# Kernel optimization log

Measured on AMD Instinct MI355X. Metric: run time of the kernel, lower is better.

The kernel has to match this reference:

```python
import jax, jax.numpy as jnp
import numpy as np

D_MODEL = 1024
NUM_HEADS = 16
D_K = D_MODEL // NUM_HEADS
SCALE = float(np.sqrt(D_K))


def setup_inputs() -> dict:
    key = jax.random.key(0)
    ks = jax.random.split(key, 11)
    B, S, D = 4, 2048, D_MODEL
    w_std = 1.0 / np.sqrt(D)
    inp = {
        "query": jax.random.normal(ks[0], (B, S, D), jnp.float32),
        "key": jax.random.normal(ks[1], (B, S, D), jnp.float32),
        "value": jax.random.normal(ks[2], (B, S, D), jnp.float32),
        "wq": jax.random.normal(ks[3], (D, D), jnp.float32) * w_std,
        "bq": jax.random.normal(ks[4], (D,), jnp.float32) * w_std,
        "wk": jax.random.normal(ks[5], (D, D), jnp.float32) * w_std,
        "bk": jax.random.normal(ks[6], (D,), jnp.float32) * w_std,
        "wv": jax.random.normal(ks[7], (D, D), jnp.float32) * w_std,
        "bv": jax.random.normal(ks[8], (D,), jnp.float32) * w_std,
        "wo": jax.random.normal(ks[9], (D, D), jnp.float32) * w_std,
        "bo": jax.random.normal(ks[10], (D,), jnp.float32) * w_std,
    }
    return inp


def reference(query, key, value, wq, bq, wk, bk, wv, bv, wo, bo):
    B, Sq, D = query.shape
    H, dk = NUM_HEADS, D_K
    # linear projections (weights stored as [in, out])
    q = query @ wq + bq
    k = key @ wk + bk
    v = value @ wv + bv
    # [B, H, S, d_k]
    q = q.reshape(B, Sq, H, dk).transpose(0, 2, 1, 3)
    k = k.reshape(B, -1, H, dk).transpose(0, 2, 1, 3)
    v = v.reshape(B, -1, H, dk).transpose(0, 2, 1, 3)
    # full attention scores [B, H, Sq, Sk]
    att = jnp.einsum("bhqd,bhkd->bhqk", q, k) / SCALE
    att = jax.nn.softmax(att, axis=-1)
    out = jnp.einsum("bhqk,bhkd->bhqd", att, v)
    out = out.transpose(0, 2, 1, 3).reshape(B, Sq, D)
    return out @ wo + bo
```

## Files before the change

### kernel.cpp

```cpp
#include <hip/hip_runtime.h>


typedef _Float16 fp16;
typedef fp16  fp16x8 __attribute__((ext_vector_type(8)));
typedef fp16  fp16x4 __attribute__((ext_vector_type(4)));
typedef float f32x4  __attribute__((ext_vector_type(4)));

#define NROWS 8192
#define DM    1024
#define SEQ   2048
#define DK    64
#define LOG2E 1.44269504088896340736f
#define QSCALE (0.125f * LOG2E)

__device__ __forceinline__ f32x4 mfma16x16(fp16x8 a, fp16x8 b, f32x4 c) {
    return __builtin_amdgcn_mfma_f32_16x16x32_f16(a, b, c, 0, 0, 0);
}

__device__ __forceinline__ void gload16(const void* g, void* l) {
    __builtin_amdgcn_global_load_lds(
        (const __attribute__((address_space(1))) void*)g,
        (__attribute__((address_space(3))) void*)l, 16, 0, 0);
}

__global__ __launch_bounds__(256) void cast_fp16_kernel(
    const float* __restrict__ x0, const float* __restrict__ x1,
    const float* __restrict__ x2,
    fp16* __restrict__ y0, fp16* __restrict__ y1, fp16* __restrict__ y2,
    int n4) {
    const int z = blockIdx.y;
    const float* x = (z == 0) ? x0 : (z == 1) ? x1 : x2;
    fp16*       y = (z == 0) ? y0 : (z == 1) ? y1 : y2;
    int i = blockIdx.x * 256 + threadIdx.x;
    if (i >= n4) return;
    const float4 v = ((const float4*)x)[i];
    fp16x4 o;
    o[0] = (fp16)v.x; o[1] = (fp16)v.y; o[2] = (fp16)v.z; o[3] = (fp16)v.w;
    ((fp16x4*)y)[i] = o;
}

__global__ __launch_bounds__(256) void transpose_w_kernel(
    const float* __restrict__ w0, const float* __restrict__ w1,
    const float* __restrict__ w2, const float* __restrict__ w3,
    fp16* __restrict__ t0, fp16* __restrict__ t1,
    fp16* __restrict__ t2, fp16* __restrict__ t3) {
    const int z = blockIdx.z;
    const float* W = (z == 0) ? w0 : (z == 1) ? w1 : (z == 2) ? w2 : w3;
    fp16*       T = (z == 0) ? t0 : (z == 1) ? t1 : (z == 2) ? t2 : t3;
    __shared__ float tile[32][33];
    const int tx = threadIdx.x, ty = threadIdx.y;
    const int bx = blockIdx.x * 32, by = blockIdx.y * 32;
#pragma unroll
    for (int j = 0; j < 4; ++j)
        tile[ty + 8 * j][tx] = W[(size_t)(by + ty + 8 * j) * DM + bx + tx];
    __syncthreads();
#pragma unroll
    for (int j = 0; j < 4; ++j)
        T[(size_t)(bx + ty + 8 * j) * DM + by + tx] = (fp16)tile[tx][ty + 8 * j];
}

__global__ __launch_bounds__(256) void gemm_qkv_kernel(
    const fp16* __restrict__ Xq, const fp16* __restrict__ Xk,
    const fp16* __restrict__ Xv,
    const fp16* __restrict__ Wq, const fp16* __restrict__ Wk,
    const fp16* __restrict__ Wv,
    const float* __restrict__ bq, const float* __restrict__ bk,
    const float* __restrict__ bv,
    fp16* __restrict__ Qb, fp16* __restrict__ Kb, fp16* __restrict__ Vtg) {
    const int i = blockIdx.x;
    const int xcd = i & 7, r = i >> 3;
    const int z = r >> 6, rr = r & 63;
    const int m0 = (xcd * 8 + (rr >> 3)) * 128;
    const int n0 = (rr & 7) * 128;

    const fp16* __restrict__ A = (z == 0) ? Xq : (z == 1) ? Xk : Xv;
    const fp16* __restrict__ B = (z == 0) ? Wq : (z == 1) ? Wk : Wv;
    const float* __restrict__ bias = (z == 0) ? bq : (z == 1) ? bk : bv;
    fp16* __restrict__ outp = (z == 0) ? Qb : (z == 1) ? Kb : Vtg;
    const float oscale = (z == 0) ? QSCALE : 1.0f;

    const int tid = threadIdx.x;
    const int lane = tid & 63;
    const int w = tid >> 6;
    const int wr = w >> 1, wc = w & 1;
    const int li = lane & 15, lg = lane >> 4;
    const int lrow = lane >> 3;
    const int lch  = (lane & 7) ^ lrow;

    __shared__ fp16 At[128 * 64];
    __shared__ fp16 Bt[128 * 64];

    f32x4 acc[4][4] = {};

    for (int k0 = 0; k0 < DM; k0 += 64) {
        __syncthreads();
#pragma unroll
        for (int it = 0; it < 4; ++it) {
            int R = (w * 4 + it) * 8 + lrow;
            gload16(&A[(size_t)(m0 + R) * DM + k0 + lch * 8], &At[(w * 4 + it) * 512]);
            gload16(&B[(size_t)(n0 + R) * DM + k0 + lch * 8], &Bt[(w * 4 + it) * 512]);
        }
        __syncthreads();
        fp16x8 af[4][2], bfr[4][2];
#pragma unroll
        for (int mf = 0; mf < 4; ++mf)
#pragma unroll
            for (int ks = 0; ks < 2; ++ks)
                af[mf][ks] = *(const fp16x8*)&At[(wr * 64 + mf * 16 + li) * 64 +
                                                 (((ks * 4 + lg) ^ (li & 7)) * 8)];
#pragma unroll
        for (int nf = 0; nf < 4; ++nf)
#pragma unroll
            for (int ks = 0; ks < 2; ++ks)
                bfr[nf][ks] = *(const fp16x8*)&Bt[(wc * 64 + nf * 16 + li) * 64 +
                                                  (((ks * 4 + lg) ^ (li & 7)) * 8)];
#pragma unroll
        for (int ks = 0; ks < 2; ++ks)
#pragma unroll
            for (int mf = 0; mf < 4; ++mf)
#pragma unroll
                for (int nf = 0; nf < 4; ++nf)
                    acc[mf][nf] = mfma16x16(af[mf][ks], bfr[nf][ks], acc[mf][nf]);
    }
#pragma unroll
    for (int nf = 0; nf < 4; ++nf) {
        int col = n0 + wc * 64 + nf * 16 + li;
        float bv_ = bias[col];
        if (z == 2) {
#pragma unroll
            for (int mf = 0; mf < 4; ++mf) {
                int rowb = m0 + wr * 64 + mf * 16 + lg * 4;
                fp16x4 pk;
#pragma unroll
                for (int r2 = 0; r2 < 4; ++r2)
                    pk[r2] = (fp16)(acc[mf][nf][r2] + bv_);
                size_t o = ((size_t)(rowb >> 11) * 1024 + col) * SEQ + (rowb & 2047);
                *(fp16x4*)&outp[o] = pk;
            }
        } else {
#pragma unroll
            for (int mf = 0; mf < 4; ++mf)
#pragma unroll
                for (int r2 = 0; r2 < 4; ++r2) {
                    int row = m0 + wr * 64 + mf * 16 + lg * 4 + r2;
                    outp[(size_t)row * DM + col] = (fp16)((acc[mf][nf][r2] + bv_) * oscale);
                }
        }
    }
}

__global__ __launch_bounds__(256) void gemm_out_kernel(
    const fp16* __restrict__ A, const fp16* __restrict__ B,
    const float* __restrict__ bias, float* __restrict__ outp) {
    const int i = blockIdx.x;
    const int xcd = i & 7, r = i >> 3;
    const int m0 = (xcd * 8 + (r >> 4)) * 128;
    const int n0 = (r & 15) * 64;

    const int tid = threadIdx.x;
    const int lane = tid & 63;
    const int w = tid >> 6;
    const int wr = w >> 1, wc = w & 1;
    const int li = lane & 15, lg = lane >> 4;
    const int lrow = lane >> 3;
    const int lch  = (lane & 7) ^ lrow;

    __shared__ fp16 At[128 * 64];
    __shared__ fp16 Bt[64 * 64];

    f32x4 acc[4][2] = {};

    for (int k0 = 0; k0 < DM; k0 += 64) {
        __syncthreads();
#pragma unroll
        for (int it = 0; it < 4; ++it) {
            int R = (w * 4 + it) * 8 + lrow;
            gload16(&A[(size_t)(m0 + R) * DM + k0 + lch * 8], &At[(w * 4 + it) * 512]);
            if (it < 2) {
                int Rb = (w * 2 + it) * 8 + lrow;
                gload16(&B[(size_t)(n0 + Rb) * DM + k0 + lch * 8], &Bt[(w * 2 + it) * 512]);
            }
        }
        __syncthreads();
        fp16x8 af[4][2], bfr[2][2];
#pragma unroll
        for (int mf = 0; mf < 4; ++mf)
#pragma unroll
            for (int ks = 0; ks < 2; ++ks)
                af[mf][ks] = *(const fp16x8*)&At[(wr * 64 + mf * 16 + li) * 64 +
                                                 (((ks * 4 + lg) ^ (li & 7)) * 8)];
#pragma unroll
        for (int nf = 0; nf < 2; ++nf)
#pragma unroll
            for (int ks = 0; ks < 2; ++ks)
                bfr[nf][ks] = *(const fp16x8*)&Bt[(wc * 32 + nf * 16 + li) * 64 +
                                                  (((ks * 4 + lg) ^ (li & 7)) * 8)];
#pragma unroll
        for (int ks = 0; ks < 2; ++ks)
#pragma unroll
            for (int mf = 0; mf < 4; ++mf)
#pragma unroll
                for (int nf = 0; nf < 2; ++nf)
                    acc[mf][nf] = mfma16x16(af[mf][ks], bfr[nf][ks], acc[mf][nf]);
    }
#pragma unroll
    for (int nf = 0; nf < 2; ++nf) {
        int col = n0 + wc * 32 + nf * 16 + li;
        float bv_ = bias[col];
#pragma unroll
        for (int mf = 0; mf < 4; ++mf)
#pragma unroll
            for (int r2 = 0; r2 < 4; ++r2) {
                int row = m0 + wr * 64 + mf * 16 + lg * 4 + r2;
                outp[(size_t)row * DM + col] = acc[mf][nf][r2] + bv_;
            }
    }
}

__global__ __launch_bounds__(512) void attn_kernel(
    const fp16* __restrict__ Qb, const fp16* __restrict__ Kb,
    const fp16* __restrict__ Vtg, fp16* __restrict__ Of) {
    const int tid = threadIdx.x;
    const int lane = tid & 63;
    const int w = tid >> 6;
    const int li = lane & 15, lg = lane >> 4;

    int L = blockIdx.x;
    L = (L & 7) * 64 + (L >> 3);
    const int qt = L & 7, bh = L >> 3;
    const int b = bh >> 4, h = bh & 15;
    const size_t rowQ = (size_t)b * SEQ + (size_t)qt * 256;
    const int c0 = h * DK;

    __shared__ fp16 Kt[2][64 * 64];
    __shared__ fp16 Vt[2][64 * 64];
    __shared__ fp16 Pl[8][32 * 64];

    fp16x8 qf[2][2];
#pragma unroll
    for (int mf = 0; mf < 2; ++mf)
#pragma unroll
        for (int ks = 0; ks < 2; ++ks)
            qf[mf][ks] = *(const fp16x8*)&Qb[(rowQ + w * 32 + mf * 16 + li) * DM +
                                             c0 + ks * 32 + lg * 8];

    fp16x8 ones;
#pragma unroll
    for (int j = 0; j < 8; ++j) ones[j] = (fp16)1.0f;

    f32x4 oacc[2][4] = {};
    f32x4 lacc[2] = {};

    const int sr = tid >> 3, sc = tid & 7;
    const int ssl = sc ^ (sr & 7);
    fp16x8 rk, rv;
    rk = *(const fp16x8*)&Kb[((size_t)b * SEQ + sr) * DM + c0 + sc * 8];
    rv = *(const fp16x8*)&Vtg[((size_t)bh * 64 + sr) * SEQ + sc * 8];
    *(fp16x8*)&Kt[0][sr * 64 + ssl * 8] = rk;
    *(fp16x8*)&Vt[0][sr * 64 + ssl * 8] = rv;
    __syncthreads();

    for (int kt = 0; kt < SEQ / 64; ++kt) {
        const int cur = kt & 1;
        const bool more = (kt + 1 < SEQ / 64);
        if (more) {
            rk = *(const fp16x8*)&Kb[((size_t)b * SEQ + (kt + 1) * 64 + sr) * DM + c0 + sc * 8];
            rv = *(const fp16x8*)&Vtg[((size_t)bh * 64 + sr) * SEQ + (kt + 1) * 64 + sc * 8];
        }

        f32x4 s[4][2] = {};
        __builtin_amdgcn_s_setprio(1);
#pragma unroll
        for (int nf = 0; nf < 4; ++nf)
#pragma unroll
            for (int ks = 0; ks < 2; ++ks) {
                fp16x8 kf = *(const fp16x8*)&Kt[cur][(nf * 16 + li) * 64 +
                                                     (((ks * 4 + lg) ^ (li & 7)) * 8)];
#pragma unroll
                for (int mf = 0; mf < 2; ++mf)
                    s[nf][mf] = mfma16x16(kf, qf[mf][ks], s[nf][mf]);
            }
        __builtin_amdgcn_s_setprio(0);

#pragma unroll
        for (int mf = 0; mf < 2; ++mf) {
            fp16x4 pk[4];
#pragma unroll
            for (int nf = 0; nf < 4; ++nf)
#pragma unroll
                for (int r = 0; r < 4; ++r)
                    pk[nf][r] = (fp16)__builtin_amdgcn_exp2f(s[nf][mf][r]);
            int row = mf * 16 + li;
#pragma unroll
            for (int nf = 0; nf < 4; ++nf) {
                int sl = (nf * 2 + (lg >> 1)) ^ (li & 7);
                *(fp16x4*)&Pl[w][row * 64 + sl * 8 + (lg & 1) * 4] = pk[nf];
            }
        }

        __builtin_amdgcn_s_setprio(1);
#pragma unroll
        for (int ks = 0; ks < 2; ++ks) {
            fp16x8 pf[2];
#pragma unroll
            for (int mf = 0; mf < 2; ++mf) {
                pf[mf] = *(const fp16x8*)&Pl[w][(mf * 16 + li) * 64 +
                                                (((ks * 4 + lg) ^ (li & 7)) * 8)];
                lacc[mf] = mfma16x16(pf[mf], ones, lacc[mf]);
            }
#pragma unroll
            for (int nf = 0; nf < 4; ++nf) {
                fp16x8 vf = *(const fp16x8*)&Vt[cur][(nf * 16 + li) * 64 +
                                                     (((ks * 4 + lg) ^ (li & 7)) * 8)];
#pragma unroll
                for (int mf = 0; mf < 2; ++mf)
                    oacc[mf][nf] = mfma16x16(pf[mf], vf, oacc[mf][nf]);
            }
        }
        __builtin_amdgcn_s_setprio(0);

        if (more) {
            *(fp16x8*)&Kt[cur ^ 1][sr * 64 + ssl * 8] = rk;
            *(fp16x8*)&Vt[cur ^ 1][sr * 64 + ssl * 8] = rv;
            __syncthreads();
        }
    }

#pragma unroll
    for (int mf = 0; mf < 2; ++mf) {
#pragma unroll
        for (int r = 0; r < 4; ++r) {
            float linv = 1.0f / lacc[mf][r];
            size_t row = rowQ + w * 32 + mf * 16 + lg * 4 + r;
#pragma unroll
            for (int nf = 0; nf < 4; ++nf) {
                int col = c0 + nf * 16 + li;
                Of[row * DM + col] = (fp16)(oacc[mf][nf][r] * linv);
            }
        }
    }
}

extern "C" void kernel_launch(void* const* d_in, const int* in_sizes, int n_in,
                              void* d_out, int out_size, void* d_ws, size_t ws_size,
                              hipStream_t stream) {
    const float* query = (const float*)d_in[0];
    const float* key   = (const float*)d_in[1];
    const float* value = (const float*)d_in[2];
    const float* wq    = (const float*)d_in[3];
    const float* bq    = (const float*)d_in[4];
    const float* wk    = (const float*)d_in[5];
    const float* bk    = (const float*)d_in[6];
    const float* wv    = (const float*)d_in[7];
    const float* bv    = (const float*)d_in[8];
    const float* wo    = (const float*)d_in[9];
    const float* bo    = (const float*)d_in[10];

    char* ws = (char*)d_ws;
    const size_t SZX = (size_t)NROWS * DM * 2;
    const size_t SZW = (size_t)DM * DM * 2;
    fp16* Xq  = (fp16*)(ws);
    fp16* Xk  = (fp16*)(ws + SZX);
    fp16* Xv  = (fp16*)(ws + 2 * SZX);
    fp16* Wtq = (fp16*)(ws + 3 * SZX);
    fp16* Wtk = (fp16*)(ws + 3 * SZX + SZW);
    fp16* Wtv = (fp16*)(ws + 3 * SZX + 2 * SZW);
    fp16* Wto = (fp16*)(ws + 3 * SZX + 3 * SZW);
    fp16* Qb  = (fp16*)(ws + 3 * SZX + 4 * SZW);
    fp16* Kb  = (fp16*)(ws + 4 * SZX + 4 * SZW);
    fp16* Vtg = (fp16*)(ws + 5 * SZX + 4 * SZW);
    fp16* Of  = Xq;

    const int n4 = NROWS * DM / 4;
    const dim3 bT(32, 8);

    cast_fp16_kernel<<<dim3(8192, 3), 256, 0, stream>>>(
        query, key, value, Xq, Xk, Xv, n4);
    transpose_w_kernel<<<dim3(32, 32, 4), bT, 0, stream>>>(
        wq, wk, wv, wo, Wtq, Wtk, Wtv, Wto);
    gemm_qkv_kernel<<<1536, 256, 0, stream>>>(
        Xq, Xk, Xv, Wtq, Wtk, Wtv, bq, bk, bv, Qb, Kb, Vtg);
    attn_kernel<<<512, 512, 0, stream>>>(Qb, Kb, Vtg, Of);
    gemm_out_kernel<<<1024, 256, 0, stream>>>(Of, Wto, bo, (float*)d_out);
}
```

Before: 212.2 us.

## Enlarge QKV GEMM tiles to 256x256 with double-buffered LDS prefetch pipeline

The QKV projection GEMM moves from 128x128 tiles with 4 waves to 256x256 tiles with 8 waves and 384 blocks. Global-to-LDS loads for the next K-step are interleaved with the MFMA phases of the current step through double buffering. Barriers, explicit waitcnts and setprio are added to overlap memory with compute. This is meant to raise operand reuse and hide load latency, at the cost of higher register and LDS use (128KB shared per block) and fewer blocks than the 256-CU device can fully balance.

Result: slower. 227.3 us (+7.2%).

```diff
diff --git a/kernel.cpp b/kernel.cpp
--- a/kernel.cpp
+++ b/kernel.cpp
@@ -59,7 +59,7 @@
         T[(size_t)(bx + ty + 8 * j) * DM + by + tx] = (fp16)tile[tx][ty + 8 * j];
 }
 
-__global__ __launch_bounds__(256) void gemm_qkv_kernel(
+__global__ __launch_bounds__(512, 2) void gemm_qkv_kernel(
     const fp16* __restrict__ Xq, const fp16* __restrict__ Xk,
     const fp16* __restrict__ Xv,
     const fp16* __restrict__ Wq, const fp16* __restrict__ Wk,
@@ -68,10 +68,10 @@
     const float* __restrict__ bv,
     fp16* __restrict__ Qb, fp16* __restrict__ Kb, fp16* __restrict__ Vtg) {
     const int i = blockIdx.x;
-    const int xcd = i & 7, r = i >> 3;
-    const int z = r >> 6, rr = r & 63;
-    const int m0 = (xcd * 8 + (rr >> 3)) * 128;
-    const int n0 = (rr & 7) * 128;
+    const int xcd = i & 7, j = i >> 3;
+    const int nt = j & 3, mloc = (j >> 2) & 3, z = j >> 4;
+    const int m0 = (xcd * 4 + mloc) * 256;
+    const int n0 = nt * 256;
 
     const fp16* __restrict__ A = (z == 0) ? Xq : (z == 1) ? Xk : Xv;
     const fp16* __restrict__ B = (z == 0) ? Wq : (z == 1) ? Wk : Wv;
@@ -82,54 +82,83 @@
     const int tid = threadIdx.x;
     const int lane = tid & 63;
     const int w = tid >> 6;
-    const int wr = w >> 1, wc = w & 1;
+    const int wr = w >> 2, wc = w & 3;
     const int li = lane & 15, lg = lane >> 4;
-    const int lrow = lane >> 3;
-    const int lch  = (lane & 7) ^ lrow;
-
-    __shared__ fp16 At[128 * 64];
-    __shared__ fp16 Bt[128 * 64];
-
-    f32x4 acc[4][4] = {};
-
-    for (int k0 = 0; k0 < DM; k0 += 64) {
-        __syncthreads();
-#pragma unroll
-        for (int it = 0; it < 4; ++it) {
-            int R = (w * 4 + it) * 8 + lrow;
-            gload16(&A[(size_t)(m0 + R) * DM + k0 + lch * 8], &At[(w * 4 + it) * 512]);
-            gload16(&B[(size_t)(n0 + R) * DM + k0 + lch * 8], &Bt[(w * 4 + it) * 512]);
-        }
-        __syncthreads();
-        fp16x8 af[4][2], bfr[4][2];
-#pragma unroll
-        for (int mf = 0; mf < 4; ++mf)
-#pragma unroll
-            for (int ks = 0; ks < 2; ++ks)
-                af[mf][ks] = *(const fp16x8*)&At[(wr * 64 + mf * 16 + li) * 64 +
-                                                 (((ks * 4 + lg) ^ (li & 7)) * 8)];
-#pragma unroll
-        for (int nf = 0; nf < 4; ++nf)
-#pragma unroll
-            for (int ks = 0; ks < 2; ++ks)
-                bfr[nf][ks] = *(const fp16x8*)&Bt[(wc * 64 + nf * 16 + li) * 64 +
-                                                  (((ks * 4 + lg) ^ (li & 7)) * 8)];
-#pragma unroll
-        for (int ks = 0; ks < 2; ++ks)
-#pragma unroll
-            for (int mf = 0; mf < 4; ++mf)
-#pragma unroll
-                for (int nf = 0; nf < 4; ++nf)
-                    acc[mf][nf] = mfma16x16(af[mf][ks], bfr[nf][ks], acc[mf][nf]);
-    }
+    const int srow = lane >> 3;
+    const int sch  = (lane & 7) ^ srow;
+
+    __shared__ fp16 Ab[2][256 * 64];
+    __shared__ fp16 Bb[2][256 * 64];
+
+    f32x4 acc[8][4] = {};
+
+#define STAGE(t, q)                                                          \
+    {                                                                        \
+        const int rowb_ = ((q) & 3) * 64 + w * 8;                            \
+        if ((q) < 4)                                                         \
+            gload16(&A[(size_t)(m0 + rowb_ + srow) * DM + (t) * 64 + sch * 8],\
+                    &Ab[(t) & 1][rowb_ * 64]);                               \
+        else                                                                 \
+            gload16(&B[(size_t)(n0 + rowb_ + srow) * DM + (t) * 64 + sch * 8],\
+                    &Bb[(t) & 1][rowb_ * 64]);                               \
+    }
+
+#pragma unroll
+    for (int q = 0; q < 8; ++q) STAGE(0, q);
+    asm volatile("s_waitcnt vmcnt(0)" ::: "memory");
+    __syncthreads();
+
+    for (int it = 0; it < 8; ++it) {
+#pragma unroll
+        for (int grp = 0; grp < 2; ++grp) {
+            const int T = it * 2 + grp;
+            const int g = T & 1;
+            const int S = T + 1;
+            fp16x8 bfr[4];
+#pragma unroll
+            for (int p = 0; p < 4; ++p) {
+                const int ks = p >> 1, mh = p & 1;
+                fp16x8 af[4];
+#pragma unroll
+                for (int m4 = 0; m4 < 4; ++m4) {
+                    int mf = mh * 4 + m4;
+                    af[m4] = *(const fp16x8*)&Ab[g][(wr * 128 + mf * 16 + li) * 64 +
+                                                    (((ks * 4 + lg) ^ (li & 7)) * 8)];
+                }
+                if (mh == 0) {
+#pragma unroll
+                    for (int nf = 0; nf < 4; ++nf)
+                        bfr[nf] = *(const fp16x8*)&Bb[g][(wc * 64 + nf * 16 + li) * 64 +
+                                                         (((ks * 4 + lg) ^ (li & 7)) * 8)];
+                }
+                if (S < 16) { STAGE(S, p * 2); STAGE(S, p * 2 + 1); }
+                __builtin_amdgcn_s_barrier();
+                asm volatile("s_waitcnt lgkmcnt(0)" ::: "memory");
+                __builtin_amdgcn_sched_barrier(0);
+                __builtin_amdgcn_s_setprio(1);
+#pragma unroll
+                for (int m4 = 0; m4 < 4; ++m4)
+#pragma unroll
+                    for (int nf = 0; nf < 4; ++nf)
+                        acc[mh * 4 + m4][nf] =
+                            mfma16x16(af[m4], bfr[nf], acc[mh * 4 + m4][nf]);
+                __builtin_amdgcn_s_setprio(0);
+                if (p == 3)
+                    asm volatile("s_waitcnt vmcnt(0)" ::: "memory");
+                __builtin_amdgcn_s_barrier();
+            }
+        }
+    }
+#undef STAGE
+
 #pragma unroll
     for (int nf = 0; nf < 4; ++nf) {
         int col = n0 + wc * 64 + nf * 16 + li;
         float bv_ = bias[col];
         if (z == 2) {
 #pragma unroll
-            for (int mf = 0; mf < 4; ++mf) {
-                int rowb = m0 + wr * 64 + mf * 16 + lg * 4;
+            for (int mf = 0; mf < 8; ++mf) {
+                int rowb = m0 + wr * 128 + mf * 16 + lg * 4;
                 fp16x4 pk;
 #pragma unroll
                 for (int r2 = 0; r2 < 4; ++r2)
@@ -139,10 +168,10 @@
             }
         } else {
 #pragma unroll
-            for (int mf = 0; mf < 4; ++mf)
+            for (int mf = 0; mf < 8; ++mf)
 #pragma unroll
                 for (int r2 = 0; r2 < 4; ++r2) {
-                    int row = m0 + wr * 64 + mf * 16 + lg * 4 + r2;
+                    int row = m0 + wr * 128 + mf * 16 + lg * 4 + r2;
                     outp[(size_t)row * DM + col] = (fp16)((acc[mf][nf][r2] + bv_) * oscale);
                 }
         }
@@ -378,7 +407,7 @@
         query, key, value, Xq, Xk, Xv, n4);
     transpose_w_kernel<<<dim3(32, 32, 4), bT, 0, stream>>>(
         wq, wk, wv, wo, Wtq, Wtk, Wtv, Wto);
-    gemm_qkv_kernel<<<1536, 256, 0, stream>>>(
+    gemm_qkv_kernel<<<384, 512, 0, stream>>>(
         Xq, Xk, Xv, Wtq, Wtk, Wtv, bq, bk, bv, Qb, Kb, Vtg);
     attn_kernel<<<512, 512, 0, stream>>>(Qb, Kb, Vtg, Of);
     gemm_out_kernel<<<1024, 256, 0, stream>>>(Of, Wto, bo, (float*)d_out);
```
